# Performance work log

Hardware: AMD Instinct MI355X
Metric: run time of the kernel (lower is better)

Reference implementation:

```python
import jax, jax.numpy as jnp
import numpy as np
from jax import lax

RATIOS = jnp.array([0.5, 1.0, 2.0], dtype=jnp.float32)
SCALES = jnp.array([8.0, 16.0, 32.0], dtype=jnp.float32)
IOU_THR = 0.5
BATCH_SIZE = 32            # module-level constant in the source
POS_RATIO = 1.0 / 3.0      # positive_ratio in the source


def _generate_anchors(fh, fw, ih, iw):
    """Vectorized version of RPN.generate_anchors. Returns (A,4) x1y1x2y2 anchors
    and an (A,) inside-image mask (static shapes; mask replaces boolean filtering)."""
    xs = iw / fw
    ys = ih / fh
    xc = (jnp.arange(fw, dtype=jnp.float32) + 0.5) * xs
    yc = (jnp.arange(fh, dtype=jnp.float32) + 0.5) * ys
    gx, gy = jnp.meshgrid(xc, yc, indexing='ij')
    centers = jnp.stack([gx.ravel(), gy.ravel()], axis=1)          # (fh*fw, 2)
    h = jnp.sqrt(SCALES[None, :] ** 2 / RATIOS[:, None]) * ys       # (3,3)
    w = h * RATIOS[:, None] * xs / ys
    wh = jnp.stack([w.ravel(), h.ravel()], axis=1)                  # (9, 2)
    lo = centers[:, None, :] - wh[None, :, :] / 2
    hi = centers[:, None, :] + wh[None, :, :] / 2
    anchors = jnp.concatenate([lo, hi], axis=2).reshape(-1, 4)      # (A, 4)
    inside = ((anchors[:, 0] >= 0) & (anchors[:, 1] >= 0) &
              (anchors[:, 2] <= iw) & (anchors[:, 3] <= ih))
    return anchors, inside


def _iou_matrix(anchors, gts):
    """Pairwise IoU between (A,4) and (G,4) corner boxes -> (A,G). Vectorizes the
    nested python loop in the original."""
    x1 = jnp.maximum(anchors[:, None, 0], gts[None, :, 0])
    y1 = jnp.maximum(anchors[:, None, 1], gts[None, :, 1])
    x2 = jnp.minimum(anchors[:, None, 2], gts[None, :, 2])
    y2 = jnp.minimum(anchors[:, None, 3], gts[None, :, 3])
    inter = jnp.maximum(x2 - x1, 0.0) * jnp.maximum(y2 - y1, 0.0)
    area_a = (anchors[:, 2] - anchors[:, 0]) * (anchors[:, 3] - anchors[:, 1])
    area_g = (gts[:, 2] - gts[:, 0]) * (gts[:, 3] - gts[:, 1])
    union = area_a[:, None] + area_g[None, :] - inter
    return jnp.where(inter > 0, inter / union, 0.0)


def _conv(x, w, b):
    return lax.conv_general_dilated(x, w, (1, 1), 'SAME',
                                    dimension_numbers=('NHWC', 'HWIO', 'NHWC')) + b


def setup_inputs() -> dict:
    key = jax.random.key(0)
    ks = jax.random.split(key, 11)
    B, H, W, C = 8, 64, 64, 512
    IMG = 1024
    std = 0.05  # keras RandomNormal default stddev
    features = jax.random.normal(ks[0], (B, H, W, C), jnp.float32)
    # 8 rows of boxes; rows 2..7 are the object boxes used by the RPN (x1,y1,x2,y2)
    xy = jax.random.uniform(ks[1], (8, 2), jnp.float32) * (IMG * 0.7)
    wh = jax.random.uniform(ks[2], (8, 2), jnp.float32) * (IMG * 0.2) + 16.0
    ground_truths = jnp.concatenate([xy, xy + wh], axis=1)
    return {
        'features': features,
        'ground_truths': ground_truths,
        'conv1_w': jax.random.normal(ks[3], (3, 3, C, 512), jnp.float32) * std,
        'conv1_b': jnp.zeros((512,), jnp.float32),
        'reg_w': jax.random.normal(ks[4], (1, 1, 512, 72), jnp.float32) * std,
        'reg_b': jnp.zeros((72,), jnp.float32),
        'cls_w': jax.random.normal(ks[5], (1, 1, 512, 9), jnp.float32) * std,
        'cls_b': jnp.zeros((9,), jnp.float32),
        'lmk_w': jax.random.normal(ks[6], (1, 1, 512, 54), jnp.float32) * std,
        'lmk_b': jnp.zeros((54,), jnp.float32),
        'img_h': IMG,
        'img_w': IMG,
    }


def reference(features, ground_truths, conv1_w, conv1_b, reg_w, reg_b,
              cls_w, cls_b, lmk_w, lmk_b, img_h, img_w):
    B, H, W, C = features.shape
    anchors, inside = _generate_anchors(H, W, float(img_h), float(img_w))
    A = anchors.shape[0]
    gts = ground_truths[2:]                                   # (6,4)
    ious = _iou_matrix(anchors, gts)                          # (A,6)
    ious = jnp.where(inside[:, None], ious, -1.0)             # outside anchors never match

    best_iou = ious.max(axis=1)
    best_idx = ious.argmax(axis=1)
    gt_best = ious.max(axis=0)
    is_best = ((ious == gt_best[None, :]) & (gt_best[None, :] > -1.0)).any(axis=1)
    labels = jnp.where((best_iou >= IOU_THR) | is_best, 1, 0)
    labels = jnp.where(inside, labels, -1)

    # balanced subsampling (np.random.choice in the original -> rank-of-random trick)
    num_pos = int(POS_RATIO * BATCH_SIZE)
    num_neg = BATCH_SIZE - num_pos
    r = jax.random.uniform(jax.random.key(42), (A,), jnp.float32)

    def keep(mask, n):
        kv = jnp.where(mask, r, jnp.inf)
        order = jnp.argsort(kv)
        rank = jnp.zeros(A, jnp.int32).at[order].set(jnp.arange(A, dtype=jnp.int32))
        return mask & (rank < n)

    pos = keep(labels == 1, num_pos)
    neg = keep(labels == 0, num_neg)
    labels = jnp.where(pos, 1, jnp.where(neg, 0, -1)).astype(jnp.float32)

    eps = jnp.finfo(jnp.float32).eps
    wa = jnp.maximum(anchors[:, 2] - anchors[:, 0], eps)
    ha = jnp.maximum(anchors[:, 3] - anchors[:, 1], eps)
    xa = anchors[:, 0] + wa / 2
    ya = anchors[:, 1] + ha / 2
    mg = gts[best_idx]                                        # (A,4) matched gt
    wg = mg[:, 2] - mg[:, 0]
    hg = mg[:, 3] - mg[:, 1]
    xg = mg[:, 0] + wg / 2
    yg = mg[:, 1] + hg / 2
    deltas = jnp.stack([(xg - xa) / wa, (yg - ya) / ha,
                        jnp.log(wg / wa), jnp.log(hg / ha)], axis=1)
    offsets = jnp.where(pos[:, None], deltas, 0.0)            # (A,4)

    # conv heads on backbone features
    x = jax.nn.relu(_conv(features, conv1_w, conv1_b))
    anchor_deltas = _conv(x, reg_w, reg_b)                    # (B,H,W,72)
    scores = jax.nn.sigmoid(_conv(x, cls_w, cls_b))           # (B,H,W,9)
    landmarks = _conv(x, lmk_w, lmk_b)                        # (B,H,W,54)
    return anchor_deltas, scores, landmarks, labels, offsets
```

## Files before the change

kernel.cpp:

```cpp
#include <hip/hip_runtime.h>
#include <cstdint>
#include <cstddef>


#define A_TOT 36864

typedef unsigned short ushortT;
typedef __attribute__((ext_vector_type(8))) short short8;
typedef __attribute__((ext_vector_type(4))) float f32x4;

typedef __attribute__((address_space(1))) unsigned char gbyte_t;
typedef __attribute__((address_space(3))) unsigned char lbyte_t;

__device__ __forceinline__ void gld_lds16(const void* g, void* l) {
  __builtin_amdgcn_global_load_lds((gbyte_t*)g, (lbyte_t*)l, 16, 0, 0);
}

__device__ __forceinline__ uint32_t rotl32(uint32_t v, int d) { return (v << d) | (v >> (32 - d)); }

__device__ __forceinline__ ushortT f2bf(float f) {
  uint32_t u = __float_as_uint(f);
  uint32_t r = (u + 0x7FFFu + ((u >> 16) & 1u)) >> 16;
  return (ushortT)r;
}

__device__ __forceinline__ uint32_t f2mono(float f) {
  uint32_t b = __float_as_uint(f);
  return b ^ ((b >> 31) ? 0xFFFFFFFFu : 0x80000000u);
}
__device__ __forceinline__ float mono2f(uint32_t u) {
  uint32_t b = (u >> 31) ? (u ^ 0x80000000u) : ~u;
  return __uint_as_float(b);
}

__device__ uint32_t threefry_bits_for(uint32_t a) {
  uint32_t x0 = 0u, x1 = a;
  const uint32_t k0 = 0u, k1 = 42u;
  const uint32_t k2 = k0 ^ k1 ^ 0x1BD11BDAu;
  x0 += k0; x1 += k1;
#define TF_RND(r) { x0 += x1; x1 = rotl32(x1, (r)); x1 ^= x0; }
  TF_RND(13) TF_RND(15) TF_RND(26) TF_RND(6)
  x0 += k1; x1 += k2 + 1u;
  TF_RND(17) TF_RND(29) TF_RND(16) TF_RND(24)
  x0 += k2; x1 += k0 + 2u;
  TF_RND(13) TF_RND(15) TF_RND(26) TF_RND(6)
  x0 += k0; x1 += k1 + 3u;
  TF_RND(17) TF_RND(29) TF_RND(16) TF_RND(24)
  x0 += k1; x1 += k2 + 4u;
  TF_RND(13) TF_RND(15) TF_RND(26) TF_RND(6)
  x0 += k2; x1 += k0 + 5u;
#undef TF_RND
  return x0 ^ x1;
}

struct Anc { float x1, y1, x2, y2; bool inside; };

__device__ __forceinline__ Anc anchor_at(int a, float iw, float ih) {
  Anc A;
  {
    #pragma clang fp contract(off)
    int p = a / 9;
    int q = a - p * 9;
    int i = p >> 6;
    int j = p & 63;
    int ri = q / 3;
    int si = q - ri * 3;
    const float ratios[3] = {0.5f, 1.0f, 2.0f};
    const float scales[3] = {8.0f, 16.0f, 32.0f};
    float xs = iw / 64.0f;
    float ys = ih / 64.0f;
    float cx = ((float)i + 0.5f) * xs;
    float cy = ((float)j + 0.5f) * ys;
    float r = ratios[ri], s = scales[si];
    float h = sqrtf((s * s) / r) * ys;
    float w = h * r * xs / ys;
    A.x1 = cx - w * 0.5f;
    A.y1 = cy - h * 0.5f;
    A.x2 = cx + w * 0.5f;
    A.y2 = cy + h * 0.5f;
    A.inside = (A.x1 >= 0.0f) && (A.y1 >= 0.0f) && (A.x2 <= iw) && (A.y2 <= ih);
  }
  return A;
}

__device__ __forceinline__ float iou_one(const Anc& A, const float* g) {
  #pragma clang fp contract(off)
  float x1 = fmaxf(A.x1, g[0]);
  float y1 = fmaxf(A.y1, g[1]);
  float x2 = fminf(A.x2, g[2]);
  float y2 = fminf(A.y2, g[3]);
  float inter = fmaxf(x2 - x1, 0.0f) * fmaxf(y2 - y1, 0.0f);
  float area_a = (A.x2 - A.x1) * (A.y2 - A.y1);
  float area_g = (g[2] - g[0]) * (g[3] - g[1]);
  float un = (area_a + area_g) - inter;
  return inter > 0.0f ? (inter / un) : 0.0f;
}

__global__ __launch_bounds__(256) void labels_gtmax_kernel(
    const float* __restrict__ gtr, const int* __restrict__ pih, const int* __restrict__ piw,
    uint32_t* __restrict__ gtbest_bits) {
  __shared__ float s_gt[6][4];
  __shared__ float s_red[4][6];
  int tid = threadIdx.x;
  if (tid < 24) ((float*)s_gt)[tid] = gtr[8 + tid];
  __syncthreads();
  float iw = (float)piw[0], ih = (float)pih[0];
  int a = blockIdx.x * 256 + tid;
  Anc A = anchor_at(a, iw, ih);
  int w = tid >> 6;
  #pragma unroll
  for (int g = 0; g < 6; ++g) {
    float v = A.inside ? iou_one(A, s_gt[g]) : -1.0f;
    for (int off = 32; off > 0; off >>= 1) v = fmaxf(v, __shfl_down(v, off, 64));
    if ((tid & 63) == 0) s_red[w][g] = v;
  }
  __syncthreads();
  if (tid < 6) {
    float m = fmaxf(fmaxf(s_red[0][tid], s_red[1][tid]), fmaxf(s_red[2][tid], s_red[3][tid]));
    atomicMax(&gtbest_bits[tid], f2mono(m));
  }
}

__global__ __launch_bounds__(256) void labels_code_kernel(
    const float* __restrict__ gtr, const int* __restrict__ pih, const int* __restrict__ piw,
    const uint32_t* __restrict__ gtbest_bits, uint32_t* __restrict__ L) {
  __shared__ float s_gt[6][4];
  __shared__ float s_gb[6];
  int tid = threadIdx.x;
  if (tid < 24) ((float*)s_gt)[tid] = gtr[8 + tid];
  if (tid < 6) s_gb[tid] = mono2f(gtbest_bits[tid]);
  __syncthreads();
  float iw = (float)piw[0], ih = (float)pih[0];
  int a = blockIdx.x * 256 + tid;
  Anc A = anchor_at(a, iw, ih);
  uint32_t code;
  if (!A.inside) {
    code = 2u;
  } else {
    float best = -1.0f;
    bool isb = false;
    #pragma unroll
    for (int g = 0; g < 6; ++g) {
      float v = iou_one(A, s_gt[g]);
      best = fmaxf(best, v);
      if (v == s_gb[g] && s_gb[g] > -1.0f) isb = true;
    }
    code = (best >= 0.5f || isb) ? 1u : 0u;
  }
  uint32_t m = threefry_bits_for((uint32_t)a) >> 9;
  L[a] = (m << 2) | code;
}

__global__ __launch_bounds__(1024) void labels_select_kernel(
    const uint32_t* __restrict__ L, unsigned long long* __restrict__ Tsel) {
  __shared__ int hist[2][512];
  __shared__ unsigned long long list[2][512];
  __shared__ int lcnt[2];
  __shared__ int s_b[2], s_r[2];
  int tid = threadIdx.x;
  hist[tid >> 9][tid & 511] = 0;
  if (tid < 2) lcnt[tid] = 0;
  __syncthreads();
  for (int a = tid; a < A_TOT; a += 1024) {
    uint32_t v = L[a];
    uint32_t c = v & 3u;
    if (c < 2u) atomicAdd(&hist[c][v >> 16], 1);
  }
  __syncthreads();
  if (tid < 2) {
    int need = (tid == 1) ? 10 : 22;
    int tot = 0;
    for (int i = 0; i < 512; ++i) tot += hist[tid][i];
    int b = -1, r = 0, cum = 0;
    if (tot > need) {
      for (int i = 0; i < 512; ++i) {
        if (cum + hist[tid][i] >= need) { b = i; r = need - cum; break; }
        cum += hist[tid][i];
      }
    }
    s_b[tid] = b; s_r[tid] = r;
    if (b < 0) Tsel[tid] = ~0ull;
  }
  __syncthreads();
  for (int a = tid; a < A_TOT; a += 1024) {
    uint32_t v = L[a];
    uint32_t c = v & 3u;
    if (c < 2u && s_b[c] == (int)(v >> 16)) {
      int idx = atomicAdd(&lcnt[c], 1);
      if (idx < 512) list[c][idx] = (((unsigned long long)(v >> 2)) << 16) | (unsigned)a;
    }
  }
  __syncthreads();
  #pragma unroll
  for (int c = 0; c < 2; ++c) {
    if (s_b[c] < 0) continue;
    int n = lcnt[c] < 512 ? lcnt[c] : 512;
    if (tid < n) {
      unsigned long long k = list[c][tid];
      int rank = 1;
      for (int i = 0; i < n; ++i) rank += (list[c][i] < k) ? 1 : 0;
      if (rank == s_r[c]) Tsel[c] = k;
    }
  }
}

__global__ __launch_bounds__(256) void labels_final_kernel(
    const uint32_t* __restrict__ L, const unsigned long long* __restrict__ Tsel,
    const float* __restrict__ gtr, const int* __restrict__ pih, const int* __restrict__ piw,
    float* __restrict__ labels_out, float* __restrict__ offs_out) {
  __shared__ float s_gt[6][4];
  int tid = threadIdx.x;
  if (tid < 24) ((float*)s_gt)[tid] = gtr[8 + tid];
  __syncthreads();
  float iw = (float)piw[0], ih = (float)pih[0];
  int a = blockIdx.x * 256 + tid;
  uint32_t v = L[a];
  uint32_t code = v & 3u;
  unsigned long long K = (((unsigned long long)(v >> 2)) << 16) | (unsigned)a;
  bool pos = (code == 1u) && (K <= Tsel[1]);
  bool neg = (code == 0u) && (K <= Tsel[0]);
  labels_out[a] = pos ? 1.0f : (neg ? 0.0f : -1.0f);
  float o0 = 0.0f, o1 = 0.0f, o2 = 0.0f, o3 = 0.0f;
  if (pos) {
    #pragma clang fp contract(off)
    Anc A = anchor_at(a, iw, ih);
    int bi = 0;
    float bv = iou_one(A, s_gt[0]);
    for (int g = 1; g < 6; ++g) {
      float vg = iou_one(A, s_gt[g]);
      if (vg > bv) { bv = vg; bi = g; }
    }
    const float eps = 1.1920928955078125e-07f;
    float wa = fmaxf(A.x2 - A.x1, eps);
    float ha = fmaxf(A.y2 - A.y1, eps);
    float xa = A.x1 + wa * 0.5f;
    float ya = A.y1 + ha * 0.5f;
    const float* g = s_gt[bi];
    float wg = g[2] - g[0];
    float hg = g[3] - g[1];
    float xg = g[0] + wg * 0.5f;
    float yg = g[1] + hg * 0.5f;
    o0 = (xg - xa) / wa;
    o1 = (yg - ya) / ha;
    o2 = logf(wg / wa);
    o3 = logf(hg / ha);
  }
  offs_out[a * 4 + 0] = o0;
  offs_out[a * 4 + 1] = o1;
  offs_out[a * 4 + 2] = o2;
  offs_out[a * 4 + 3] = o3;
}

__global__ void prep_w_kernel(const float* __restrict__ w, ushortT* __restrict__ Wt) {
  int idx = blockIdx.x * 256 + threadIdx.x;
  if (idx >= 9 * 512 * 512) return;
  int ic = idx & 511;
  int t = idx >> 9;
  int oc = t & 511;
  int kk = t >> 9;
  Wt[idx] = f2bf(w[((size_t)kk * 512 + ic) * 512 + oc]);
}

__global__ void prep_feat_kernel(const float* __restrict__ feat, ushortT* __restrict__ featbf,
                                 ushortT* __restrict__ zrow) {
  int idx = blockIdx.x * 256 + threadIdx.x;
  if (idx < 2097152) {
    const float4 f0 = *(const float4*)(feat + (size_t)idx * 8);
    const float4 f1 = *(const float4*)(feat + (size_t)idx * 8 + 4);
    short8 o;
    o[0] = (short)f2bf(f0.x); o[1] = (short)f2bf(f0.y);
    o[2] = (short)f2bf(f0.z); o[3] = (short)f2bf(f0.w);
    o[4] = (short)f2bf(f1.x); o[5] = (short)f2bf(f1.y);
    o[6] = (short)f2bf(f1.z); o[7] = (short)f2bf(f1.w);
    *(short8*)(featbf + (size_t)idx * 8) = o;
  }
  if (idx < 4096) {
    *(short8*)(zrow + (size_t)idx * 8) = (short8){0, 0, 0, 0, 0, 0, 0, 0};
  }
}

__global__ void pack_w_kernel(const float* __restrict__ reg_w, const float* __restrict__ cls_w,
                              const float* __restrict__ lmk_w, const float* __restrict__ reg_b,
                              const float* __restrict__ cls_b, const float* __restrict__ lmk_b,
                              ushortT* __restrict__ Wh, float* __restrict__ bias_all,
                              uint32_t* __restrict__ gtbest_bits) {
  int idx = blockIdx.x * 256 + threadIdx.x;
  if (idx < 144 * 512) {
    int c = idx >> 9, ic = idx & 511;
    float v = 0.0f;
    if (c < 72) v = reg_w[ic * 72 + c];
    else if (c < 81) v = cls_w[ic * 9 + (c - 72)];
    else if (c < 135) v = lmk_w[ic * 54 + (c - 81)];
    Wh[idx] = f2bf(v);
  }
  if (blockIdx.x == 0) {
    int t = threadIdx.x;
    if (t < 144) {
      float bv = 0.0f;
      if (t < 72) bv = reg_b[t];
      else if (t < 81) bv = cls_b[t - 72];
      else if (t < 135) bv = lmk_b[t - 81];
      bias_all[t] = bv;
    }
    if (t < 6) gtbest_bits[t] = f2mono(-1.0f);
  }
}

__global__ __launch_bounds__(256) void conv3x3_mfma_kernel(
    const ushortT* __restrict__ featbf, const ushortT* __restrict__ zrow,
    const ushortT* __restrict__ Wt, const float* __restrict__ bias,
    ushortT* __restrict__ xbf) {
  __shared__ __align__(16) char smem[2][32768];
  const int tid = threadIdx.x;
  const int lane = tid & 63;
  const int w = tid >> 6;
  const int kgrp = lane >> 4;
  const int ln15 = lane & 15;
  const int wm = (w >> 1) * 64;
  const int wn = (w & 1) * 64;
  const int wn16 = wn >> 4;

  const int lin = blockIdx.x + 4 * blockIdx.y;
  const int swz = (lin & 7) * 128 + (lin >> 3);
  const int oc0 = (swz & 3) * 128;
  const int mb = swz >> 2;
  const int b = mb >> 5;
  const int y0 = (mb & 31) * 2;

  const int bn15 = lane & 15;
  const int bic = ((lane >> 4) & 3) * 8;

  f32x4 acc[4][4];
  #pragma unroll
  for (int i = 0; i < 4; ++i)
    #pragma unroll
    for (int j = 0; j < 4; ++j) acc[i][j] = (f32x4){0.f, 0.f, 0.f, 0.f};
  const short8 zv = (short8){0, 0, 0, 0, 0, 0, 0, 0};

  auto stageA = [&](int t, int bsel) {
    int ic0 = (t / 3) * 32;
    int dy = (t % 3) - 1;
    char* Ab = smem[bsel];
    #pragma unroll
    for (int i = 0; i < 2; ++i) {
      int c = w + i * 4;
      int h = c >> 2, q = c & 3;
      int ysrc = y0 + h + dy;
      bool vy = (unsigned)ysrc < 64u;
      const ushortT* rowbase = vy ? (featbf + ((size_t)((b * 64 + ysrc) * 64)) * 512) : zrow;
      const ushortT* src = rowbase + (size_t)(q * 16 + bn15) * 512 + ic0 + bic;
      gld_lds16(src, Ab + c * 1024);
    }
  };
  auto issueB = [&](int t, int bsel) {
    int ic0 = (t / 3) * 32;
    int ky = t % 3;
    char* Bb = smem[bsel] + 8192;
    #pragma unroll
    for (int i = 0; i < 6; ++i) {
      int c = w + i * 4;
      int kxr = c >> 3, cc = c & 7;
      int kk = ky * 3 + kxr;
      int n = cc * 16 + bn15;
      const ushortT* src = Wt + ((size_t)(kk * 512 + oc0 + n)) * 512 + ic0 + bic;
      gld_lds16(src, Bb + kxr * 8192 + cc * 1024);
    }
  };
  auto computeT = [&](int t, int bsel) {
    const char* Ab = smem[bsel];
    const char* Bb = smem[bsel] + 8192;
    int dy = (t % 3) - 1;
    int rowv = y0 + (wm >> 6) + dy;
    if ((unsigned)rowv >= 64u) return;
    #pragma unroll
    for (int kx = 0; kx < 3; ++kx) {
      const int dx = kx - 1;
      short8 bfr[4];
      #pragma unroll
      for (int j = 0; j < 4; ++j)
        bfr[j] = *(const short8*)(Bb + kx * 8192 + (wn16 + j) * 1024 + kgrp * 256 + ln15 * 16);
      short8 afr[4];
      #pragma unroll
      for (int i = 0; i < 4; ++i) {
        int xin = i * 16 + ln15 + dx;
        bool ok = (unsigned)xin < 64u;
        int p_in = wm + (ok ? xin : 0);
        short8 v = *(const short8*)(Ab + (p_in >> 4) * 1024 + kgrp * 256 + (p_in & 15) * 16);
        afr[i] = ok ? v : zv;
      }
      #pragma unroll
      for (int i = 0; i < 4; ++i)
        #pragma unroll
        for (int j = 0; j < 4; ++j)
          acc[i][j] = __builtin_amdgcn_mfma_f32_16x16x32_bf16(afr[i], bfr[j], acc[i][j], 0, 0, 0);
    }
  };

  stageA(0, 0);
  issueB(0, 0);
  __syncthreads();

  int buf = 0;
  for (int t = 0; t < 48; ++t) {
    if (t < 47) { stageA(t + 1, buf ^ 1); issueB(t + 1, buf ^ 1); }
    computeT(t, buf);
    __syncthreads();
    buf ^= 1;
  }

  #pragma unroll
  for (int j = 0; j < 4; ++j) {
    int n = oc0 + wn + j * 16 + ln15;
    float bv = bias[n];
    #pragma unroll
    for (int i = 0; i < 4; ++i) {
      int mrow = mb * 128 + wm + i * 16 + kgrp * 4;
      #pragma unroll
      for (int r = 0; r < 4; ++r) {
        float v = fmaxf(acc[i][j][r] + bv, 0.0f);
        xbf[(size_t)(mrow + r) * 512 + n] = f2bf(v);
      }
    }
  }
}

__global__ __launch_bounds__(256) void conv3x3_mfma_fb_kernel(
    const float* __restrict__ feat, const ushortT* __restrict__ Wt,
    const float* __restrict__ bias, ushortT* __restrict__ xbf) {
  __shared__ __align__(16) char smem[2][32768];
  const int tid = threadIdx.x;
  const int lane = tid & 63;
  const int w = tid >> 6;
  const int kgrp = lane >> 4;
  const int ln15 = lane & 15;
  const int wm = (w >> 1) * 64;
  const int wn = (w & 1) * 64;
  const int wn16 = wn >> 4;
  const int lin = blockIdx.x + 4 * blockIdx.y;
  const int swz = (lin & 7) * 128 + (lin >> 3);
  const int oc0 = (swz & 3) * 128;
  const int mb = swz >> 2;
  const int b = mb >> 5;
  const int y0 = (mb & 31) * 2;
  const int sp0 = (tid >> 6) * 16 + (tid & 15);
  const int sk0 = ((tid >> 4) & 3) * 8;
  const int bn15 = lane & 15;
  const int bic = ((lane >> 4) & 3) * 8;

  f32x4 acc[4][4];
  #pragma unroll
  for (int i = 0; i < 4; ++i)
    #pragma unroll
    for (int j = 0; j < 4; ++j) acc[i][j] = (f32x4){0.f, 0.f, 0.f, 0.f};
  const short8 zv = (short8){0, 0, 0, 0, 0, 0, 0, 0};

  auto issueA = [&](int t, float4* aL) {
    int ic0 = (t / 3) * 32;
    int dy = (t % 3) - 1;
    #pragma unroll
    for (int h = 0; h < 2; ++h) {
      int p = sp0 + h * 64;
      int ys = y0 + (p >> 6) + dy;
      ys = ys < 0 ? 0 : (ys > 63 ? 63 : ys);
      const float* sp = feat + ((size_t)((b * 64 + ys) * 64 + (p & 63))) * 512 + ic0 + sk0;
      aL[h * 2 + 0] = *(const float4*)sp;
      aL[h * 2 + 1] = *(const float4*)(sp + 4);
    }
  };
  auto issueB = [&](int t, int bsel) {
    int ic0 = (t / 3) * 32;
    int ky = t % 3;
    char* Bb = smem[bsel] + 8192;
    #pragma unroll
    for (int i = 0; i < 6; ++i) {
      int c = w + i * 4;
      int kxr = c >> 3, cc = c & 7;
      int kk = ky * 3 + kxr;
      int n = cc * 16 + bn15;
      const ushortT* src = Wt + ((size_t)(kk * 512 + oc0 + n)) * 512 + ic0 + bic;
      gld_lds16(src, Bb + kxr * 8192 + cc * 1024);
    }
  };
  auto writeA = [&](const float4* aL, int bsel) {
    char* Ab = smem[bsel];
    #pragma unroll
    for (int h = 0; h < 2; ++h) {
      float4 f0 = aL[h * 2 + 0], f1 = aL[h * 2 + 1];
      short8 o;
      o[0] = (short)f2bf(f0.x); o[1] = (short)f2bf(f0.y);
      o[2] = (short)f2bf(f0.z); o[3] = (short)f2bf(f0.w);
      o[4] = (short)f2bf(f1.x); o[5] = (short)f2bf(f1.y);
      o[6] = (short)f2bf(f1.z); o[7] = (short)f2bf(f1.w);
      *(short8*)(Ab + h * 4096 + tid * 16) = o;
    }
  };
  auto computeT = [&](int t, int bsel) {
    const char* Ab = smem[bsel];
    const char* Bb = smem[bsel] + 8192;
    int dy = (t % 3) - 1;
    int rowv = y0 + (wm >> 6) + dy;
    if ((unsigned)rowv >= 64u) return;
    #pragma unroll
    for (int kx = 0; kx < 3; ++kx) {
      const int dx = kx - 1;
      short8 bfr[4];
      #pragma unroll
      for (int j = 0; j < 4; ++j)
        bfr[j] = *(const short8*)(Bb + kx * 8192 + (wn16 + j) * 1024 + kgrp * 256 + ln15 * 16);
      short8 afr[4];
      #pragma unroll
      for (int i = 0; i < 4; ++i) {
        int xin = i * 16 + ln15 + dx;
        bool ok = (unsigned)xin < 64u;
        int p_in = wm + (ok ? xin : 0);
        short8 v = *(const short8*)(Ab + (p_in >> 4) * 1024 + kgrp * 256 + (p_in & 15) * 16);
        afr[i] = ok ? v : zv;
      }
      #pragma unroll
      for (int i = 0; i < 4; ++i)
        #pragma unroll
        for (int j = 0; j < 4; ++j)
          acc[i][j] = __builtin_amdgcn_mfma_f32_16x16x32_bf16(afr[i], bfr[j], acc[i][j], 0, 0, 0);
    }
  };

  {
    float4 aL[4];
    issueA(0, aL);
    issueB(0, 0);
    writeA(aL, 0);
  }
  __syncthreads();

  int buf = 0;
  for (int t = 0; t < 48; ++t) {
    float4 aN[4];
    if (t < 47) { issueA(t + 1, aN); issueB(t + 1, buf ^ 1); }
    computeT(t, buf);
    if (t < 47) writeA(aN, buf ^ 1);
    __syncthreads();
    buf ^= 1;
  }

  #pragma unroll
  for (int j = 0; j < 4; ++j) {
    int n = oc0 + wn + j * 16 + ln15;
    float bv = bias[n];
    #pragma unroll
    for (int i = 0; i < 4; ++i) {
      int mrow = mb * 128 + wm + i * 16 + kgrp * 4;
      #pragma unroll
      for (int r = 0; r < 4; ++r) {
        float v = fmaxf(acc[i][j][r] + bv, 0.0f);
        xbf[(size_t)(mrow + r) * 512 + n] = f2bf(v);
      }
    }
  }
}

__global__ __launch_bounds__(256) void heads_mfma_kernel(
    const ushortT* __restrict__ x, const ushortT* __restrict__ Wh,
    const float* __restrict__ bias_all,
    float* __restrict__ out_deltas, float* __restrict__ out_scores, float* __restrict__ out_lmk) {
  __shared__ __align__(16) char smem[2][17408];
  const int tid = threadIdx.x;
  const int lane = tid & 63;
  const int w = tid >> 6;
  const int kgrp = lane >> 4;
  const int ln15 = lane & 15;
  const int m0 = blockIdx.x * 128;
  const int bn15 = lane & 15;
  const int bic = ((lane >> 4) & 3) * 8;

  f32x4 acc[2][9];
  #pragma unroll
  for (int i = 0; i < 2; ++i)
    #pragma unroll
    for (int j = 0; j < 9; ++j) acc[i][j] = (f32x4){0.f, 0.f, 0.f, 0.f};

  auto stage = [&](int t, int bsel) {
    int k0 = t * 32;
    char* Ab = smem[bsel];
    char* Bb = smem[bsel] + 8192;
    #pragma unroll
    for (int i = 0; i < 2; ++i) {
      int cc = w + i * 4;
      int p = cc * 16 + bn15;
      gld_lds16(x + ((size_t)(m0 + p)) * 512 + k0 + bic, Ab + cc * 1024);
    }
    for (int c = w; c < 9; c += 4) {
      int n = c * 16 + bn15;
      gld_lds16(Wh + ((size_t)n) * 512 + k0 + bic, Bb + c * 1024);
    }
  };
  auto computeH = [&](int bsel) {
    const char* Ab = smem[bsel];
    const char* Bb = smem[bsel] + 8192;
    short8 afr[2], bfr[9];
    #pragma unroll
    for (int i = 0; i < 2; ++i)
      afr[i] = *(const short8*)(Ab + (w * 2 + i) * 1024 + kgrp * 256 + ln15 * 16);
    #pragma unroll
    for (int j = 0; j < 9; ++j)
      bfr[j] = *(const short8*)(Bb + j * 1024 + kgrp * 256 + ln15 * 16);
    #pragma unroll
    for (int i = 0; i < 2; ++i)
      #pragma unroll
      for (int j = 0; j < 9; ++j)
        acc[i][j] = __builtin_amdgcn_mfma_f32_16x16x32_bf16(afr[i], bfr[j], acc[i][j], 0, 0, 0);
  };

  stage(0, 0);
  __syncthreads();
  int buf = 0;
  for (int t = 0; t < 16; ++t) {
    if (t < 15) stage(t + 1, buf ^ 1);
    computeH(buf);
    __syncthreads();
    buf ^= 1;
  }

  #pragma unroll
  for (int j = 0; j < 9; ++j) {
    int c = j * 16 + ln15;
    float bv = bias_all[c];
    #pragma unroll
    for (int i = 0; i < 2; ++i) {
      int mrow = m0 + w * 32 + i * 16 + kgrp * 4;
      #pragma unroll
      for (int r = 0; r < 4; ++r) {
        size_t m = (size_t)(mrow + r);
        float v = acc[i][j][r] + bv;
        if (c < 72) out_deltas[m * 72 + c] = v;
        else if (c < 81) out_scores[m * 9 + (c - 72)] = 1.0f / (1.0f + expf(-v));
        else if (c < 135) out_lmk[m * 54 + (c - 81)] = v;
      }
    }
  }
}

extern "C" void kernel_launch(void* const* d_in, const int* in_sizes, int n_in,
                              void* d_out, int out_size, void* d_ws, size_t ws_size,
                              hipStream_t stream) {
  const float* feat    = (const float*)d_in[0];
  const float* gtr     = (const float*)d_in[1];
  const float* conv1_w = (const float*)d_in[2];
  const float* conv1_b = (const float*)d_in[3];
  const float* reg_w   = (const float*)d_in[4];
  const float* reg_b   = (const float*)d_in[5];
  const float* cls_w   = (const float*)d_in[6];
  const float* cls_b   = (const float*)d_in[7];
  const float* lmk_w   = (const float*)d_in[8];
  const float* lmk_b   = (const float*)d_in[9];
  const int*   pih     = (const int*)d_in[10];
  const int*   piw     = (const int*)d_in[11];

  float* out = (float*)d_out;
  float* deltas = out;
  float* scores = out + 2359296;
  float* lmk    = out + 2654208;
  float* labels = out + 4423680;
  float* offs   = out + 4460544;

  ushortT*  Wt          = (ushortT*)d_ws;
  ushortT*  Wh          = (ushortT*)((char*)d_ws + 4718592);
  float*    bias_all    = (float*)((char*)d_ws + 4866048);
  uint32_t* gtbest_bits = (uint32_t*)((char*)d_ws + 4866688);
  unsigned long long* Tsel = (unsigned long long*)((char*)d_ws + 4866752);
  ushortT*  xbf         = (ushortT*)((char*)d_ws + 4866816);
  uint32_t* L           = (uint32_t*)((char*)d_ws + 38421248);
  ushortT*  featbf      = (ushortT*)((char*)d_ws + 38568704);
  ushortT*  zrow        = (ushortT*)((char*)d_ws + 72123136);

  const bool use_bf16A = ws_size >= 72188672ull;

  prep_w_kernel<<<9216, 256, 0, stream>>>(conv1_w, Wt);
  pack_w_kernel<<<288, 256, 0, stream>>>(reg_w, cls_w, lmk_w, reg_b, cls_b, lmk_b,
                                         Wh, bias_all, gtbest_bits);

  dim3 gconv(4, 256);
  if (use_bf16A) {
    prep_feat_kernel<<<8192, 256, 0, stream>>>(feat, featbf, zrow);
    conv3x3_mfma_kernel<<<gconv, 256, 0, stream>>>(featbf, zrow, Wt, conv1_b, xbf);
  } else {
    conv3x3_mfma_fb_kernel<<<gconv, 256, 0, stream>>>(feat, Wt, conv1_b, xbf);
  }

  heads_mfma_kernel<<<256, 256, 0, stream>>>(xbf, Wh, bias_all, deltas, scores, lmk);

  labels_gtmax_kernel<<<144, 256, 0, stream>>>(gtr, pih, piw, gtbest_bits);
  labels_code_kernel<<<144, 256, 0, stream>>>(gtr, pih, piw, gtbest_bits, L);
  labels_select_kernel<<<1, 1024, 0, stream>>>(L, Tsel);
  labels_final_kernel<<<144, 256, 0, stream>>>(L, Tsel, gtr, pih, piw, labels, offs);
}
```

Before: 265.7 us.

## Merge prep kernels and halve conv output-channel tile to raise occupancy

The three preprocessing kernels (weight transpose, feature bf16 cast, head weight packing) become one launch, removing two kernel launches. The main 3x3 conv kernel's output-channel tile drops from 128 to 64 per block, with half the accumulators and B-tile LDS per block. The grid doubles to 8x256 and launch bounds request 4 blocks per CU. This trades more redundant A-tile loads, since each feature tile is now fetched by 8 blocks instead of 4, for higher occupancy and better latency hiding.

```diff
diff --git a/kernel.cpp b/kernel.cpp
--- a/kernel.cpp
+++ b/kernel.cpp
@@ -251,20 +251,23 @@
   offs_out[a * 4 + 3] = o3;
 }
 
-__global__ void prep_w_kernel(const float* __restrict__ w, ushortT* __restrict__ Wt) {
+__global__ void prep_all_kernel(const float* __restrict__ w, const float* __restrict__ feat,
+                                const float* __restrict__ reg_w, const float* __restrict__ cls_w,
+                                const float* __restrict__ lmk_w, const float* __restrict__ reg_b,
+                                const float* __restrict__ cls_b, const float* __restrict__ lmk_b,
+                                ushortT* __restrict__ Wt, ushortT* __restrict__ featbf,
+                                ushortT* __restrict__ zrow, ushortT* __restrict__ Wh,
+                                float* __restrict__ bias_all, uint32_t* __restrict__ gtbest_bits,
+                                int do_feat) {
   int idx = blockIdx.x * 256 + threadIdx.x;
-  if (idx >= 9 * 512 * 512) return;
-  int ic = idx & 511;
-  int t = idx >> 9;
-  int oc = t & 511;
-  int kk = t >> 9;
-  Wt[idx] = f2bf(w[((size_t)kk * 512 + ic) * 512 + oc]);
-}
-
-__global__ void prep_feat_kernel(const float* __restrict__ feat, ushortT* __restrict__ featbf,
-                                 ushortT* __restrict__ zrow) {
-  int idx = blockIdx.x * 256 + threadIdx.x;
-  if (idx < 2097152) {
+  {
+    int ic = idx & 511;
+    int t = idx >> 9;
+    int oc = t & 511;
+    int kk = t >> 9;
+    Wt[idx] = f2bf(w[((size_t)kk * 512 + ic) * 512 + oc]);
+  }
+  if (do_feat && idx < 2097152) {
     const float4 f0 = *(const float4*)(feat + (size_t)idx * 8);
     const float4 f1 = *(const float4*)(feat + (size_t)idx * 8 + 4);
     short8 o;
@@ -274,18 +277,7 @@
     o[6] = (short)f2bf(f1.z); o[7] = (short)f2bf(f1.w);
     *(short8*)(featbf + (size_t)idx * 8) = o;
   }
-  if (idx < 4096) {
-    *(short8*)(zrow + (size_t)idx * 8) = (short8){0, 0, 0, 0, 0, 0, 0, 0};
-  }
-}
-
-__global__ void pack_w_kernel(const float* __restrict__ reg_w, const float* __restrict__ cls_w,
-                              const float* __restrict__ lmk_w, const float* __restrict__ reg_b,
-                              const float* __restrict__ cls_b, const float* __restrict__ lmk_b,
-                              ushortT* __restrict__ Wh, float* __restrict__ bias_all,
-                              uint32_t* __restrict__ gtbest_bits) {
-  int idx = blockIdx.x * 256 + threadIdx.x;
-  if (idx < 144 * 512) {
+  if (idx < 73728) {
     int c = idx >> 9, ic = idx & 511;
     float v = 0.0f;
     if (c < 72) v = reg_w[ic * 72 + c];
@@ -293,48 +285,48 @@
     else if (c < 135) v = lmk_w[ic * 54 + (c - 81)];
     Wh[idx] = f2bf(v);
   }
-  if (blockIdx.x == 0) {
-    int t = threadIdx.x;
-    if (t < 144) {
-      float bv = 0.0f;
-      if (t < 72) bv = reg_b[t];
-      else if (t < 81) bv = cls_b[t - 72];
-      else if (t < 135) bv = lmk_b[t - 81];
-      bias_all[t] = bv;
-    }
-    if (t < 6) gtbest_bits[t] = f2mono(-1.0f);
-  }
-}
-
-__global__ __launch_bounds__(256) void conv3x3_mfma_kernel(
+  if (do_feat && idx < 4096) {
+    *(short8*)(zrow + (size_t)idx * 8) = (short8){0, 0, 0, 0, 0, 0, 0, 0};
+  }
+  if (idx < 144) {
+    float bv = 0.0f;
+    if (idx < 72) bv = reg_b[idx];
+    else if (idx < 81) bv = cls_b[idx - 72];
+    else if (idx < 135) bv = lmk_b[idx - 81];
+    bias_all[idx] = bv;
+  }
+  if (idx < 6) gtbest_bits[idx] = f2mono(-1.0f);
+}
+
+__global__ __launch_bounds__(256, 4) void conv3x3_mfma_kernel(
     const ushortT* __restrict__ featbf, const ushortT* __restrict__ zrow,
     const ushortT* __restrict__ Wt, const float* __restrict__ bias,
     ushortT* __restrict__ xbf) {
-  __shared__ __align__(16) char smem[2][32768];
+  __shared__ __align__(16) char smem[2][20480];
   const int tid = threadIdx.x;
   const int lane = tid & 63;
   const int w = tid >> 6;
   const int kgrp = lane >> 4;
   const int ln15 = lane & 15;
   const int wm = (w >> 1) * 64;
-  const int wn = (w & 1) * 64;
+  const int wn = (w & 1) * 32;
   const int wn16 = wn >> 4;
 
-  const int lin = blockIdx.x + 4 * blockIdx.y;
-  const int swz = (lin & 7) * 128 + (lin >> 3);
-  const int oc0 = (swz & 3) * 128;
-  const int mb = swz >> 2;
+  const int lin = blockIdx.x + 8 * blockIdx.y;
+  const int swz = (lin & 7) * 256 + (lin >> 3);
+  const int oc0 = (swz & 7) * 64;
+  const int mb = swz >> 3;
   const int b = mb >> 5;
   const int y0 = (mb & 31) * 2;
 
   const int bn15 = lane & 15;
   const int bic = ((lane >> 4) & 3) * 8;
 
-  f32x4 acc[4][4];
+  f32x4 acc[4][2];
   #pragma unroll
   for (int i = 0; i < 4; ++i)
     #pragma unroll
-    for (int j = 0; j < 4; ++j) acc[i][j] = (f32x4){0.f, 0.f, 0.f, 0.f};
+    for (int j = 0; j < 2; ++j) acc[i][j] = (f32x4){0.f, 0.f, 0.f, 0.f};
   const short8 zv = (short8){0, 0, 0, 0, 0, 0, 0, 0};
 
   auto stageA = [&](int t, int bsel) {
@@ -357,13 +349,13 @@
     int ky = t % 3;
     char* Bb = smem[bsel] + 8192;
     #pragma unroll
-    for (int i = 0; i < 6; ++i) {
+    for (int i = 0; i < 3; ++i) {
       int c = w + i * 4;
-      int kxr = c >> 3, cc = c & 7;
+      int kxr = c >> 2, cc = c & 3;
       int kk = ky * 3 + kxr;
       int n = cc * 16 + bn15;
       const ushortT* src = Wt + ((size_t)(kk * 512 + oc0 + n)) * 512 + ic0 + bic;
-      gld_lds16(src, Bb + kxr * 8192 + cc * 1024);
+      gld_lds16(src, Bb + kxr * 4096 + cc * 1024);
     }
   };
   auto computeT = [&](int t, int bsel) {
@@ -375,10 +367,10 @@
     #pragma unroll
     for (int kx = 0; kx < 3; ++kx) {
       const int dx = kx - 1;
-      short8 bfr[4];
-      #pragma unroll
-      for (int j = 0; j < 4; ++j)
-        bfr[j] = *(const short8*)(Bb + kx * 8192 + (wn16 + j) * 1024 + kgrp * 256 + ln15 * 16);
+      short8 bfr[2];
+      #pragma unroll
+      for (int j = 0; j < 2; ++j)
+        bfr[j] = *(const short8*)(Bb + kx * 4096 + (wn16 + j) * 1024 + kgrp * 256 + ln15 * 16);
       short8 afr[4];
       #pragma unroll
       for (int i = 0; i < 4; ++i) {
@@ -391,7 +383,7 @@
       #pragma unroll
       for (int i = 0; i < 4; ++i)
         #pragma unroll
-        for (int j = 0; j < 4; ++j)
+        for (int j = 0; j < 2; ++j)
           acc[i][j] = __builtin_amdgcn_mfma_f32_16x16x32_bf16(afr[i], bfr[j], acc[i][j], 0, 0, 0);
     }
   };
@@ -409,7 +401,7 @@
   }
 
   #pragma unroll
-  for (int j = 0; j < 4; ++j) {
+  for (int j = 0; j < 2; ++j) {
     int n = oc0 + wn + j * 16 + ln15;
     float bv = bias[n];
     #pragma unroll
@@ -674,15 +666,16 @@
 
   const bool use_bf16A = ws_size >= 72188672ull;
 
-  prep_w_kernel<<<9216, 256, 0, stream>>>(conv1_w, Wt);
-  pack_w_kernel<<<288, 256, 0, stream>>>(reg_w, cls_w, lmk_w, reg_b, cls_b, lmk_b,
-                                         Wh, bias_all, gtbest_bits);
-
-  dim3 gconv(4, 256);
+  prep_all_kernel<<<9216, 256, 0, stream>>>(conv1_w, feat, reg_w, cls_w, lmk_w,
+                                            reg_b, cls_b, lmk_b, Wt, featbf, zrow,
+                                            Wh, bias_all, gtbest_bits,
+                                            use_bf16A ? 1 : 0);
+
   if (use_bf16A) {
-    prep_feat_kernel<<<8192, 256, 0, stream>>>(feat, featbf, zrow);
+    dim3 gconv(8, 256);
     conv3x3_mfma_kernel<<<gconv, 256, 0, stream>>>(featbf, zrow, Wt, conv1_b, xbf);
   } else {
+    dim3 gconv(4, 256);
     conv3x3_mfma_fb_kernel<<<gconv, 256, 0, stream>>>(feat, Wt, conv1_b, xbf);
   }
 
```

Result: slower. 300.2 us (+13.0%).
